# Optimization experiments

Hardware: AMD Instinct MI355X
Metric: run time of the kernel (lower is better)

The kernel has to match this reference:

```python
import jax, jax.numpy as jnp
import numpy as np

B = 2048
BEAMS = 4
DEPTH = 3
HID = 128
NOPS = 4


def _conv(x, w, b):
    y = jax.lax.conv_general_dilated(x, w, (1, 1), 'VALID',
                                     dimension_numbers=('NCHW', 'OIHW', 'NCHW'))
    return y + b[None, :, None, None]


def _bn(x, g, b, eps=1e-5):
    # training-mode BatchNorm2d: batch statistics over (N,H,W)
    mu = x.mean(axis=(0, 2, 3), keepdims=True)
    var = x.var(axis=(0, 2, 3), keepdims=True)
    return (x - mu) * jax.lax.rsqrt(var + eps) * g[None, :, None, None] + b[None, :, None, None]


def _avgpool2(x):
    n, c, h, w = x.shape
    x = x[:, :, :(h // 2) * 2, :(w // 2) * 2]
    return x.reshape(n, c, h // 2, 2, w // 2, 2).mean(axis=(3, 5))


def _backbone(x, cw1, cb1, g1, be1, cw2, cb2, g2, be2, cw3, cb3, g3, be3):
    x = _avgpool2(jax.nn.relu(_bn(_conv(x, cw1, cb1), g1, be1)))  # (N,32,15,15)
    x = _avgpool2(jax.nn.relu(_bn(_conv(x, cw2, cb2), g2, be2)))  # (N,32,6,6)
    x = _avgpool2(jax.nn.relu(_bn(_conv(x, cw3, cb3), g3, be3)))  # (N,32,2,2)
    return x.reshape(x.shape[0], -1)  # (N,128)


def _beam_search(h0, W_hh, b_h, E_op, W_ho, b_ho):
    # tanh-RNN router + top-k beam search over NOPS ops, DEPTH steps.
    # path[t]: (N, BEAMS, NOPS) = one_hot(selected op) * its softmax prob.
    n = h0.shape[0]
    logits0 = h0 @ W_ho + b_ho                       # (N,4)
    logp0 = jax.nn.log_softmax(logits0, axis=-1)
    probs0 = jax.nn.softmax(logits0, axis=-1)
    scores, ops = jax.lax.top_k(logp0, BEAMS)        # (N,beams)
    p = jnp.take_along_axis(probs0, ops, axis=1)
    path = [jax.nn.one_hot(ops, NOPS) * p[..., None]]
    h = jnp.tanh(h0[:, None, :] @ W_hh + E_op[ops] + b_h)  # (N,beams,128)
    for _ in range(DEPTH - 1):
        logits = h @ W_ho + b_ho                     # (N,beams,4)
        logp = jax.nn.log_softmax(logits, axis=-1)
        probs = jax.nn.softmax(logits, axis=-1)
        cand = (scores[:, :, None] + logp).reshape(n, BEAMS * NOPS)
        scores, flat = jax.lax.top_k(cand, BEAMS)
        src = flat // NOPS
        op = flat % NOPS
        probs_src = jnp.take_along_axis(probs, src[:, :, None], axis=1)
        p = jnp.take_along_axis(probs_src, op[:, :, None], axis=2)[..., 0]
        path.append(jax.nn.one_hot(op, NOPS) * p[..., None])
        h_src = jnp.take_along_axis(h, src[:, :, None], axis=1)
        h = jnp.tanh(h_src @ W_hh + E_op[op] + b_h)
    return path


def _dispatch(hid, ops, exp_w, exp_b):
    # per-row argmax-routed expert (3 Linear + Identity), gated by max prob, then ReLU
    idx = jnp.argmax(ops, axis=-1)                   # (M,)
    val = jnp.max(ops, axis=-1)                      # (M,)
    y_lin = jnp.einsum('md,edk->mek', hid, exp_w) + exp_b  # (M,3,128)
    y = jnp.concatenate([y_lin, hid[:, None, :]], axis=1)  # (M,4,128)
    sel = jnp.take_along_axis(y, idx[:, None, None], axis=1)[:, 0]
    return jax.nn.relu(sel * val[:, None])


def _forward(x, cw1, cb1, g1, be1, cw2, cb2, g2, be2, cw3, cb3, g3, be3,
             W_hh, b_h, E_op, W_ho, b_ho, exp_w, exp_b, out_w, out_b):
    h0 = _backbone(x, cw1, cb1, g1, be1, cw2, cb2, g2, be2, cw3, cb3, g3, be3)
    path = _beam_search(h0, W_hh, b_h, E_op, W_ho, b_ho)
    n = h0.shape[0]
    hid = jnp.broadcast_to(h0[:, None, :], (n, BEAMS, HID)).reshape(n * BEAMS, HID)
    for ops in path:
        hid = _dispatch(hid, ops.reshape(n * BEAMS, NOPS), exp_w, exp_b)
    return hid @ out_w + out_b                       # (n*beams, 10)


def setup_inputs():
    key = jax.random.key(0)
    ks = jax.random.split(key, 10)
    s = 0.05
    return {
        'x': jax.random.normal(ks[0], (B, 3, 32, 32), jnp.float32),
        'cw1': jax.random.normal(ks[1], (32, 3, 3, 3), jnp.float32) * s,
        'cb1': jnp.zeros((32,), jnp.float32),
        'g1': jnp.ones((32,), jnp.float32), 'be1': jnp.zeros((32,), jnp.float32),
        'cw2': jax.random.normal(ks[2], (32, 32, 3, 3), jnp.float32) * s,
        'cb2': jnp.zeros((32,), jnp.float32),
        'g2': jnp.ones((32,), jnp.float32), 'be2': jnp.zeros((32,), jnp.float32),
        'cw3': jax.random.normal(ks[3], (32, 32, 3, 3), jnp.float32) * s,
        'cb3': jnp.zeros((32,), jnp.float32),
        'g3': jnp.ones((32,), jnp.float32), 'be3': jnp.zeros((32,), jnp.float32),
        'W_hh': jax.random.normal(ks[4], (HID, HID), jnp.float32) * s,
        'b_h': jnp.zeros((HID,), jnp.float32),
        'E_op': jax.random.normal(ks[5], (NOPS, HID), jnp.float32) * s,
        'W_ho': jax.random.normal(ks[6], (HID, NOPS), jnp.float32) * s,
        'b_ho': jnp.zeros((NOPS,), jnp.float32),
        'exp_w': jax.random.normal(ks[7], (3, HID, HID), jnp.float32) * s,
        'exp_b': jnp.zeros((3, HID), jnp.float32),
        'out_w': jax.random.normal(ks[8], (HID, 10), jnp.float32) * s,
        'out_b': jnp.zeros((10,), jnp.float32),
    }


def reference(x, cw1, cb1, g1, be1, cw2, cb2, g2, be2, cw3, cb3, g3, be3,
              W_hh, b_h, E_op, W_ho, b_ho, exp_w, exp_b, out_w, out_b):
    return _forward(x, cw1, cb1, g1, be1, cw2, cb2, g2, be2, cw3, cb3, g3, be3,
                    W_hh, b_h, E_op, W_ho, b_ho, exp_w, exp_b, out_w, out_b)
```

## Files before the change

### kernel.cpp

```cpp
#include <hip/hip_runtime.h>
#include <cstdint>


static constexpr size_t O_SC    = 0;
static constexpr size_t O_W1T   = 256;
static constexpr size_t O_W2T   = 1152;
static constexpr size_t O_W3T   = 10368;
static constexpr size_t O_SCORES= 19584;
static constexpr size_t O_P0    = 27776;
static constexpr size_t O_P1    = 35968;
static constexpr size_t O_P2    = 44160;
static constexpr size_t O_OP0   = 52352;
static constexpr size_t O_OP1   = 60544;
static constexpr size_t O_OP2   = 68736;
static constexpr size_t O_SRC1  = 76928;
static constexpr size_t O_SRC2  = 85120;
static constexpr size_t O_H0    = 93312;
static constexpr size_t O_H     = 355456;
static constexpr size_t O_H2    = 1404032;
static constexpr size_t O_HIDA  = 2452608;
static constexpr size_t O_HIDB  = 3501184;
static constexpr size_t O_S1P   = 4549760;
static constexpr size_t O_S2C   = 19295360;
static constexpr size_t O_S2P   = 30371968;
static constexpr size_t O_S3C   = 32731264;
static constexpr size_t O_PART  = O_H;
static constexpr size_t O_PART2 = O_H + 131072;

__device__ __forceinline__ int swz8(int Q, int cb) {
    return cb ^ (Q & 7) ^ ((Q >> 3) & 7);
}

__global__ void prep_w(const float* __restrict__ w1, const float* __restrict__ w2,
                       const float* __restrict__ w3, float* __restrict__ w1t,
                       float* __restrict__ w2t, float* __restrict__ w3t) {
    int t = blockIdx.x * 256 + threadIdx.x;
    if (t < 864) {
        int co = t / 27, k = t % 27;
        w1t[k * 32 + co] = w1[t];
    }
    if (t < 9216) {
        int co = t / 288, rest = t % 288;
        int ci = rest / 9, tap = rest % 9;
        int k = tap * 32 + ci;
        w2t[k * 32 + co] = w2[t];
        w3t[k * 32 + co] = w3[t];
    }
}

__global__ __launch_bounds__(256) void reduce_part64(
    const float* __restrict__ part, int nblocks, float* __restrict__ part2) {
    __shared__ float red[256];
    const int b = blockIdx.x, t = threadIdx.x;
    const int c = t & 63, grp = t >> 6;
    float s = 0.f;
    for (int i = b + 64 * grp; i < nblocks; i += 256)
        s += part[(size_t)i * 64 + c];
    red[t] = s;
    __syncthreads();
    if (t < 64)
        part2[(size_t)b * 64 + t] =
            red[t] + red[64 + t] + red[128 + t] + red[192 + t];
}

__global__ __launch_bounds__(256) void finalize_stats(
    const float* __restrict__ part, int nblocks, float invcount,
    const float* __restrict__ g, const float* __restrict__ be,
    float* __restrict__ scsh) {
    __shared__ float red[256];
    const int t = threadIdx.x;
    const int c = t & 63, grp = t >> 6;
    float s = 0.f;
    for (int i = grp; i < nblocks; i += 4) s += part[(size_t)i * 64 + c];
    red[t] = s;
    __syncthreads();
    if (t < 64) red[t] = red[t] + red[64 + t] + red[128 + t] + red[192 + t];
    __syncthreads();
    if (t < 32) {
        float mean = red[t] * invcount;
        float var = red[32 + t] * invcount - mean * mean;
        float sc = g[t] * rsqrtf(var + 1e-5f);
        scsh[t] = sc;
        scsh[32 + t] = be[t] - mean * sc;
    }
}

#define CONV1_STAGE(img4, xin, t)                                              \
    for (int i = (t); i < 1024; i += 256) {                                    \
        int slot = (i & 1) * 16 + ((i & 31) >> 1);                             \
        img4[(i >> 5) * 32 + slot] =                                           \
            make_float4(xin[i], xin[1024 + i], xin[2048 + i], 0.f);            \
    }

__device__ __forceinline__ float f4c(float4 v, int ci) {
    return ci == 0 ? v.x : (ci == 1 ? v.y : v.z);
}

#define CONV1_PQUAD(img4, wb, ph, pw, y)                                       \
    {                                                                          \
        _Pragma("unroll")                                                      \
        for (int tr = 0; tr < 3; ++tr) {                                       \
            const int rb_ = (2 * (ph) + tr) * 32 + (pw);                       \
            float4 a0_[4], a1_[4];                                             \
            a0_[0] = img4[rb_ + 0];  a0_[1] = img4[rb_ + 16];                  \
            a0_[2] = img4[rb_ + 1];  a0_[3] = img4[rb_ + 17];                  \
            a1_[0] = img4[rb_ + 32]; a1_[1] = img4[rb_ + 48];                  \
            a1_[2] = img4[rb_ + 33]; a1_[3] = img4[rb_ + 49];                  \
            _Pragma("unroll")                                                  \
            for (int tc = 0; tc < 3; ++tc) {                                   \
                _Pragma("unroll")                                              \
                for (int ci = 0; ci < 3; ++ci) {                               \
                    const float* w8_ = (wb) + (ci * 9 + tr * 3 + tc) * 32;     \
                    float4 wa_ = *(const float4*)w8_;                          \
                    float4 wq_ = *(const float4*)(w8_ + 4);                    \
                    float wr_[8] = {wa_.x, wa_.y, wa_.z, wa_.w,                \
                                    wq_.x, wq_.y, wq_.z, wq_.w};               \
                    const float s00_ = f4c(a0_[tc], ci);                       \
                    const float s01_ = f4c(a0_[tc + 1], ci);                   \
                    const float s10_ = f4c(a1_[tc], ci);                       \
                    const float s11_ = f4c(a1_[tc + 1], ci);                   \
                    _Pragma("unroll")                                          \
                    for (int cc = 0; cc < 8; ++cc) {                           \
                        y[0][cc] += s00_ * wr_[cc];                            \
                        y[1][cc] += s01_ * wr_[cc];                            \
                        y[2][cc] += s10_ * wr_[cc];                            \
                        y[3][cc] += s11_ * wr_[cc];                            \
                    }                                                          \
                }                                                              \
            }                                                                  \
        }                                                                      \
    }

__global__ __launch_bounds__(256, 4) void conv1_stats_kernel(
    const float* __restrict__ x, const float* __restrict__ w1t,
    float* __restrict__ part) {
    __shared__ float4 img4[1024];
    const int n = blockIdx.x, t = threadIdx.x;
    const float* xin = x + (size_t)n * 3072;
    CONV1_STAGE(img4, xin, t)
    const int wv = t >> 6, lane = t & 63;
    const int c0s = __builtin_amdgcn_readfirstlane(wv * 8);
    const float* __restrict__ wb = w1t + c0s;
    __syncthreads();
    float sm[8] = {}, sq[8] = {};
#pragma unroll 1
    for (int j = 0; j < 4; ++j) {
        const int pp = lane + 64 * j;
        const bool pv = pp < 225;
        const int pc = pv ? pp : 0;
        const int ph = pc / 15, pw = pc % 15;
        float y[4][8] = {};
        CONV1_PQUAD(img4, wb, ph, pw, y)
        if (pv) {
#pragma unroll
            for (int q = 0; q < 4; ++q)
#pragma unroll
                for (int cc = 0; cc < 8; ++cc) {
                    float v = y[q][cc];
                    sm[cc] += v; sq[cc] += v * v;
                }
        }
    }
#pragma unroll
    for (int off = 32; off > 0; off >>= 1)
#pragma unroll
        for (int cc = 0; cc < 8; ++cc) {
            sm[cc] += __shfl_down(sm[cc], off);
            sq[cc] += __shfl_down(sq[cc], off);
        }
    if (lane == 0) {
        float* dst = part + (size_t)n * 64;
#pragma unroll
        for (int cc = 0; cc < 8; ++cc) {
            dst[c0s + cc] = sm[cc];
            dst[32 + c0s + cc] = sq[cc];
        }
    }
}

__global__ __launch_bounds__(256, 4) void conv1_apply_kernel(
    const float* __restrict__ x, const float* __restrict__ w1t,
    const float* __restrict__ scsh, float* __restrict__ s1p) {
    __shared__ float4 img4[1024];
    const int n = blockIdx.x, t = threadIdx.x;
    const float* xin = x + (size_t)n * 3072;
    CONV1_STAGE(img4, xin, t)
    const int wv = t >> 6, lane = t & 63;
    const int c0s = __builtin_amdgcn_readfirstlane(wv * 8);
    const float* __restrict__ wb = w1t + c0s;
    float scv[8], shv[8];
#pragma unroll
    for (int cc = 0; cc < 8; ++cc) {
        scv[cc] = scsh[c0s + cc];
        shv[cc] = scsh[32 + c0s + cc];
    }
    __syncthreads();
#pragma unroll 1
    for (int j = 0; j < 4; ++j) {
        const int pp = lane + 64 * j;
        const bool pv = pp < 225;
        const int pc = pv ? pp : 0;
        const int ph = pc / 15, pw = pc % 15;
        float y[4][8] = {};
        CONV1_PQUAD(img4, wb, ph, pw, y)
        if (pv) {
            float ov[8];
#pragma unroll
            for (int cc = 0; cc < 8; ++cc) {
                float sc = scv[cc], sh = shv[cc];
                float a0 = fmaxf(y[0][cc] * sc + sh, 0.f);
                float a1 = fmaxf(y[1][cc] * sc + sh, 0.f);
                float a2 = fmaxf(y[2][cc] * sc + sh, 0.f);
                float a3 = fmaxf(y[3][cc] * sc + sh, 0.f);
                ov[cc] = 0.25f * (a0 + a1 + a2 + a3);
            }
            float* dst = s1p + ((size_t)n * 225 + pc) * 32 + c0s;
            *(float4*)dst = make_float4(ov[0], ov[1], ov[2], ov[3]);
            *(float4*)(dst + 4) = make_float4(ov[4], ov[5], ov[6], ov[7]);
        }
    }
}

__global__ __launch_bounds__(256, 5) void conv2_kernel(
    const float* __restrict__ s1p, const float* __restrict__ w2t,
    float* __restrict__ s2c, float* __restrict__ part) {
    __shared__ float4 img4[1800];
    const int n = blockIdx.x, t = threadIdx.x;
    const float4* src4 = (const float4*)(s1p + (size_t)n * 7200);
    for (int i = t; i < 1800; i += 256) {
        int p = i >> 3, cb = i & 7;
        img4[(p << 3) + swz8(p, cb)] = src4[i];
    }
    const int wv = t >> 6, lane = t & 63;
    const int c0s = __builtin_amdgcn_readfirstlane(wv * 8);
    const float* __restrict__ wbase = w2t + c0s;
    int pxv[3], in0[3];
    bool val[3];
#pragma unroll
    for (int j = 0; j < 3; ++j) {
        int p = lane + 64 * j;
        val[j] = p < 169;
        int pc = val[j] ? p : 0;
        pxv[j] = pc;
        in0[j] = (pc / 13) * 15 + (pc % 13);
    }
    float y[3][8] = {};
    __syncthreads();
#pragma unroll 1
    for (int tap = 0; tap < 9; ++tap) {
        const int dp = (tap / 3) * 15 + (tap % 3);
        int qb[3], qs[3];
#pragma unroll
        for (int j = 0; j < 3; ++j) {
            int q = in0[j] + dp;
            qb[j] = q << 3;
            qs[j] = (q & 7) ^ ((q >> 3) & 7);
        }
        const float* wk = wbase + tap * 1024;
#pragma unroll
        for (int cb = 0; cb < 8; ++cb) {
            float4 v0 = img4[qb[0] + (cb ^ qs[0])];
            float4 v1 = img4[qb[1] + (cb ^ qs[1])];
            float4 v2 = img4[qb[2] + (cb ^ qs[2])];
#pragma unroll
            for (int u = 0; u < 4; ++u) {
                const float* w8 = wk + (cb * 4 + u) * 32;
                float4 wa = *(const float4*)w8;
                float4 wb = *(const float4*)(w8 + 4);
                float wreg[8] = {wa.x, wa.y, wa.z, wa.w, wb.x, wb.y, wb.z, wb.w};
                float sv[3] = {((const float*)&v0)[u], ((const float*)&v1)[u],
                               ((const float*)&v2)[u]};
#pragma unroll
                for (int j = 0; j < 3; ++j)
#pragma unroll
                    for (int cc = 0; cc < 8; ++cc)
                        y[j][cc] += sv[j] * wreg[cc];
            }
        }
    }
#pragma unroll
    for (int j = 0; j < 3; ++j)
        if (val[j]) {
            float* dst = s2c + ((size_t)n * 169 + pxv[j]) * 32 + c0s;
            *(float4*)dst = make_float4(y[j][0], y[j][1], y[j][2], y[j][3]);
            *(float4*)(dst + 4) = make_float4(y[j][4], y[j][5], y[j][6], y[j][7]);
        }
    float sm[8] = {}, sq[8] = {};
#pragma unroll
    for (int j = 0; j < 3; ++j)
        if (val[j]) {
#pragma unroll
            for (int cc = 0; cc < 8; ++cc) {
                float v = y[j][cc];
                sm[cc] += v; sq[cc] += v * v;
            }
        }
#pragma unroll
    for (int off = 32; off > 0; off >>= 1)
#pragma unroll
        for (int cc = 0; cc < 8; ++cc) {
            sm[cc] += __shfl_down(sm[cc], off);
            sq[cc] += __shfl_down(sq[cc], off);
        }
    if (lane == 0) {
        float* dst = part + (size_t)n * 64;
#pragma unroll
        for (int cc = 0; cc < 8; ++cc) {
            dst[c0s + cc] = sm[cc];
            dst[32 + c0s + cc] = sq[cc];
        }
    }
}

__global__ __launch_bounds__(256) void conv3_kernel(
    const float* __restrict__ s2p, const float* __restrict__ w3t,
    float* __restrict__ s3c, float* __restrict__ part) {
    __shared__ float4 img4[1152];
    const int n0 = blockIdx.x * 4, t = threadIdx.x;
    const float4* src4 = (const float4*)(s2p + (size_t)n0 * 1152);
    for (int i = t; i < 1152; i += 256) {
        int im = i / 288, rem = i - im * 288;
        int p = rem >> 3, cb = rem & 7;
        img4[im * 288 + (p << 3) + swz8(im * 36 + p, cb)] = src4[i];
    }
    const int wv = t >> 6, lane = t & 63;
    const int c0s = __builtin_amdgcn_readfirstlane(wv * 8);
    const float* __restrict__ wbase = w3t + c0s;
    const int im = lane >> 4, p = lane & 15;
    const int in0 = (p >> 2) * 6 + (p & 3);
    float y[8] = {};
    __syncthreads();
#pragma unroll 1
    for (int tap = 0; tap < 9; ++tap) {
        const int q = in0 + (tap / 3) * 6 + (tap % 3);
        const int P = im * 36 + q;
        const int qb = im * 288 + (q << 3);
        const int qs = (P & 7) ^ ((P >> 3) & 7);
        const float* wk = wbase + tap * 1024;
#pragma unroll
        for (int cb = 0; cb < 8; ++cb) {
            float4 v = img4[qb + (cb ^ qs)];
#pragma unroll
            for (int u = 0; u < 4; ++u) {
                const float* w8 = wk + (cb * 4 + u) * 32;
                float4 wa = *(const float4*)w8;
                float4 wb = *(const float4*)(w8 + 4);
                float wreg[8] = {wa.x, wa.y, wa.z, wa.w, wb.x, wb.y, wb.z, wb.w};
                float s = ((const float*)&v)[u];
#pragma unroll
                for (int cc = 0; cc < 8; ++cc) y[cc] += s * wreg[cc];
            }
        }
    }
    float* dst = s3c + ((size_t)(n0 + im) * 16 + p) * 32 + c0s;
    *(float4*)dst = make_float4(y[0], y[1], y[2], y[3]);
    *(float4*)(dst + 4) = make_float4(y[4], y[5], y[6], y[7]);
    float sm[8], sq[8];
#pragma unroll
    for (int cc = 0; cc < 8; ++cc) {
        sm[cc] = y[cc]; sq[cc] = y[cc] * y[cc];
    }
#pragma unroll
    for (int off = 32; off > 0; off >>= 1)
#pragma unroll
        for (int cc = 0; cc < 8; ++cc) {
            sm[cc] += __shfl_down(sm[cc], off);
            sq[cc] += __shfl_down(sq[cc], off);
        }
    if (lane == 0) {
        float* dstp = part + (size_t)blockIdx.x * 64;
#pragma unroll
        for (int cc = 0; cc < 8; ++cc) {
            dstp[c0s + cc] = sm[cc];
            dstp[32 + c0s + cc] = sq[cc];
        }
    }
}

__global__ void bn_pool2(const float* __restrict__ s2c, const float* __restrict__ scsh,
                         float* __restrict__ s2p) {
    __shared__ float bn[64];
    const int t = threadIdx.x;
    if (t < 64) bn[t] = scsh[t];
    __syncthreads();
    for (int idx = blockIdx.x * blockDim.x + t; idx < 2359296;
         idx += gridDim.x * blockDim.x) {
        const int ci = idx & 31, rest = idx >> 5;
        const int pp = rest % 36, n = rest / 36;
        const int ph = pp / 6, pw = pp % 6;
        const float* b = s2c + ((size_t)n * 169 + (2 * ph) * 13 + 2 * pw) * 32 + ci;
        const float s = bn[ci], h = bn[32 + ci];
        float a0 = fmaxf(b[0] * s + h, 0.f);
        float a1 = fmaxf(b[32] * s + h, 0.f);
        float a2 = fmaxf(b[13 * 32] * s + h, 0.f);
        float a3 = fmaxf(b[14 * 32] * s + h, 0.f);
        s2p[idx] = 0.25f * (a0 + a1 + a2 + a3);
    }
}

__global__ void bn_pool3_h0(const float* __restrict__ s3c, const float* __restrict__ scsh,
                            float* __restrict__ h0) {
    __shared__ float bn[64];
    const int t = threadIdx.x;
    if (t < 64) bn[t] = scsh[t];
    __syncthreads();
    const int idx = blockIdx.x * 256 + t;
    if (idx >= 262144) return;
    const int n = idx >> 7, rem = idx & 127;
    const int c = rem >> 2, q = rem & 3, ph = q >> 1, pw = q & 1;
    const float* b = s3c + ((size_t)n * 16 + 2 * ph * 4 + 2 * pw) * 32 + c;
    const float s = bn[c], h = bn[32 + c];
    float a0 = fmaxf(b[0] * s + h, 0.f);
    float a1 = fmaxf(b[32] * s + h, 0.f);
    float a2 = fmaxf(b[128] * s + h, 0.f);
    float a3 = fmaxf(b[160] * s + h, 0.f);
    h0[idx] = 0.25f * (a0 + a1 + a2 + a3);
}

__global__ void beam0_kernel(const float* __restrict__ h0, const float* __restrict__ Who,
                             const float* __restrict__ bho, float* __restrict__ scores,
                             int* __restrict__ op0, float* __restrict__ p0) {
    const int n = blockIdx.x, lane = threadIdx.x;
    const float* hr = h0 + (size_t)n * 128;
    float pt[4] = {};
    for (int i = lane; i < 128; i += 64) {
        float hv = hr[i];
        pt[0] += hv * Who[i * 4 + 0];
        pt[1] += hv * Who[i * 4 + 1];
        pt[2] += hv * Who[i * 4 + 2];
        pt[3] += hv * Who[i * 4 + 3];
    }
#pragma unroll
    for (int off = 32; off > 0; off >>= 1)
#pragma unroll
        for (int o = 0; o < 4; ++o) pt[o] += __shfl_down(pt[o], off);
    if (lane == 0) {
        float lg[4], e[4], probs[4], logp[4];
#pragma unroll
        for (int o = 0; o < 4; ++o) lg[o] = pt[o] + bho[o];
        float m = fmaxf(fmaxf(lg[0], lg[1]), fmaxf(lg[2], lg[3]));
        float sum = 0.f;
#pragma unroll
        for (int o = 0; o < 4; ++o) { e[o] = expf(lg[o] - m); sum += e[o]; }
        float lse = logf(sum);
#pragma unroll
        for (int o = 0; o < 4; ++o) {
            probs[o] = e[o] / sum;
            logp[o] = lg[o] - m - lse;
        }
        bool used[4] = {false, false, false, false};
        for (int slot = 0; slot < 4; ++slot) {
            int best = 0; float bv = -INFINITY;
            for (int o = 0; o < 4; ++o)
                if (!used[o] && logp[o] > bv) { bv = logp[o]; best = o; }
            used[best] = true;
            scores[n * 4 + slot] = bv;
            op0[n * 4 + slot] = best;
            p0[n * 4 + slot] = probs[best];
        }
    }
}

__global__ void beam_level(const float* __restrict__ h, const float* __restrict__ Who,
                           const float* __restrict__ bho, float* __restrict__ scores,
                           int* __restrict__ opL, float* __restrict__ pL,
                           int* __restrict__ srcL) {
    __shared__ float logits[16], cand[16], pr[16];
    const int n = blockIdx.x, l = threadIdx.x;
    const int b = l >> 4, o = (l >> 2) & 3, qt = l & 3;
    const float* hr = h + ((size_t)n * 4 + b) * 128;
    float s = 0.f;
    for (int k = qt * 32; k < qt * 32 + 32; ++k) s += hr[k] * Who[k * 4 + o];
    s += __shfl_xor(s, 1);
    s += __shfl_xor(s, 2);
    if (qt == 0) logits[b * 4 + o] = s + bho[o];
    __syncthreads();
    if (l < 4) {
        float lg[4];
#pragma unroll
        for (int o2 = 0; o2 < 4; ++o2) lg[o2] = logits[l * 4 + o2];
        float m = fmaxf(fmaxf(lg[0], lg[1]), fmaxf(lg[2], lg[3]));
        float e[4], sum = 0.f;
#pragma unroll
        for (int o2 = 0; o2 < 4; ++o2) { e[o2] = expf(lg[o2] - m); sum += e[o2]; }
        float lse = logf(sum);
        float sb = scores[n * 4 + l];
#pragma unroll
        for (int o2 = 0; o2 < 4; ++o2) {
            pr[l * 4 + o2] = e[o2] / sum;
            cand[l * 4 + o2] = sb + (lg[o2] - m - lse);
        }
    }
    __syncthreads();
    if (l == 0) {
        bool used[16];
#pragma unroll
        for (int f = 0; f < 16; ++f) used[f] = false;
        float ns[4], np[4]; int nop[4], nsrc[4];
        for (int slot = 0; slot < 4; ++slot) {
            int best = 0; float bv = -INFINITY;
            for (int f = 0; f < 16; ++f)
                if (!used[f] && cand[f] > bv) { bv = cand[f]; best = f; }
            used[best] = true;
            ns[slot] = bv; nsrc[slot] = best >> 2; nop[slot] = best & 3;
            np[slot] = pr[best];
        }
        for (int slot = 0; slot < 4; ++slot) {
            scores[n * 4 + slot] = ns[slot];
            opL[n * 4 + slot] = nop[slot];
            pL[n * 4 + slot] = np[slot];
            srcL[n * 4 + slot] = nsrc[slot];
        }
    }
}

__global__ __launch_bounds__(256) void h_update(
    const float* __restrict__ in, int mode, const int* __restrict__ srcL,
    const int* __restrict__ opL, const float* __restrict__ Whh,
    const float* __restrict__ Eop, const float* __restrict__ bh,
    float* __restrict__ out) {
    __shared__ float A[256];
    const int r0 = blockIdx.x * 2, t = threadIdx.x;
    const int row = t >> 7, j = t & 127;
    const int r = r0 + row;
    const float* src;
    if (mode == 0) src = in + (size_t)(r >> 2) * 128;
    else           src = in + (size_t)((r & ~3) + srcL[r]) * 128;
    A[t] = src[j];
    __syncthreads();
    float acc = 0.f;
#pragma unroll 8
    for (int k = 0; k < 128; ++k) acc += A[row * 128 + k] * Whh[k * 128 + j];
    out[(size_t)r * 128 + j] = tanhf(acc + Eop[opL[r] * 128 + j] + bh[j]);
}

__global__ __launch_bounds__(256) void dispatch_kernel(
    const float* __restrict__ in, int mode, const int* __restrict__ opL,
    const float* __restrict__ pL, const float* __restrict__ expw,
    const float* __restrict__ expb, float* __restrict__ out) {
    __shared__ float A[256];
    const int r0 = blockIdx.x * 2, t = threadIdx.x;
    const int row = t >> 7, j = t & 127;
    const int r = r0 + row;
    const float* src = (mode == 0) ? in + (size_t)(r >> 2) * 128
                                   : in + (size_t)r * 128;
    A[t] = src[j];
    __syncthreads();
    const int op = opL[r];
    const float p = pL[r];
    float res;
    if (op < 3) {
        const float* Bw = expw + (size_t)op * 16384;
        float acc = 0.f;
#pragma unroll 8
        for (int k = 0; k < 128; ++k) acc += A[row * 128 + k] * Bw[k * 128 + j];
        res = (acc + expb[op * 128 + j]) * p;
    } else {
        res = A[row * 128 + j] * p;
    }
    out[(size_t)r * 128 + j] = fmaxf(res, 0.f);
}

__global__ void final_kernel(const float* __restrict__ hid, const float* __restrict__ ow,
                             const float* __restrict__ ob, float* __restrict__ out) {
    const int idx = blockIdx.x * 256 + threadIdx.x;
    if (idx >= 81920) return;
    const int r = idx / 10, o = idx % 10;
    const float* hr = hid + (size_t)r * 128;
    float acc = ob[o];
#pragma unroll 8
    for (int k = 0; k < 128; ++k) acc += hr[k] * ow[k * 10 + o];
    out[idx] = acc;
}

extern "C" void kernel_launch(void* const* d_in, const int* in_sizes, int n_in,
                              void* d_out, int out_size, void* d_ws, size_t ws_size,
                              hipStream_t stream) {
    const float* x    = (const float*)d_in[0];
    const float* cw1  = (const float*)d_in[1];
    const float* g1   = (const float*)d_in[3];
    const float* be1  = (const float*)d_in[4];
    const float* cw2  = (const float*)d_in[5];
    const float* g2   = (const float*)d_in[7];
    const float* be2  = (const float*)d_in[8];
    const float* cw3  = (const float*)d_in[9];
    const float* g3   = (const float*)d_in[11];
    const float* be3  = (const float*)d_in[12];
    const float* Whh  = (const float*)d_in[13];
    const float* bh   = (const float*)d_in[14];
    const float* Eop  = (const float*)d_in[15];
    const float* Who  = (const float*)d_in[16];
    const float* bho  = (const float*)d_in[17];
    const float* expw = (const float*)d_in[18];
    const float* expb = (const float*)d_in[19];
    const float* outw = (const float*)d_in[20];
    const float* outb = (const float*)d_in[21];
    float* ws  = (float*)d_ws;
    float* out = (float*)d_out;

    prep_w<<<36, 256, 0, stream>>>(cw1, cw2, cw3, ws + O_W1T, ws + O_W2T, ws + O_W3T);

    conv1_stats_kernel<<<2048, 256, 0, stream>>>(x, ws + O_W1T, ws + O_PART);
    reduce_part64<<<64, 256, 0, stream>>>(ws + O_PART, 2048, ws + O_PART2);
    finalize_stats<<<1, 256, 0, stream>>>(ws + O_PART2, 64, 1.f / 1843200.f,
                                          g1, be1, ws + O_SC);
    conv1_apply_kernel<<<2048, 256, 0, stream>>>(x, ws + O_W1T, ws + O_SC, ws + O_S1P);
    conv2_kernel<<<2048, 256, 0, stream>>>(ws + O_S1P, ws + O_W2T, ws + O_S2C,
                                           ws + O_PART);
    reduce_part64<<<64, 256, 0, stream>>>(ws + O_PART, 2048, ws + O_PART2);
    finalize_stats<<<1, 256, 0, stream>>>(ws + O_PART2, 64, 1.f / 346112.f,
                                          g2, be2, ws + O_SC + 64);
    bn_pool2<<<2048, 256, 0, stream>>>(ws + O_S2C, ws + O_SC + 64, ws + O_S2P);
    conv3_kernel<<<512, 256, 0, stream>>>(ws + O_S2P, ws + O_W3T, ws + O_S3C,
                                          ws + O_PART);
    reduce_part64<<<64, 256, 0, stream>>>(ws + O_PART, 512, ws + O_PART2);
    finalize_stats<<<1, 256, 0, stream>>>(ws + O_PART2, 64, 1.f / 32768.f,
                                          g3, be3, ws + O_SC + 128);
    bn_pool3_h0<<<1024, 256, 0, stream>>>(ws + O_S3C, ws + O_SC + 128, ws + O_H0);

    beam0_kernel<<<2048, 64, 0, stream>>>(ws + O_H0, Who, bho, ws + O_SCORES,
                                          (int*)(ws + O_OP0), ws + O_P0);
    h_update<<<4096, 256, 0, stream>>>(ws + O_H0, 0, (int*)(ws + O_SRC2),
                                       (int*)(ws + O_OP0), Whh, Eop, bh, ws + O_H);
    beam_level<<<2048, 64, 0, stream>>>(ws + O_H, Who, bho, ws + O_SCORES,
                                        (int*)(ws + O_OP1), ws + O_P1,
                                        (int*)(ws + O_SRC1));
    h_update<<<4096, 256, 0, stream>>>(ws + O_H, 1, (int*)(ws + O_SRC1),
                                       (int*)(ws + O_OP1), Whh, Eop, bh, ws + O_H2);
    beam_level<<<2048, 64, 0, stream>>>(ws + O_H2, Who, bho, ws + O_SCORES,
                                        (int*)(ws + O_OP2), ws + O_P2,
                                        (int*)(ws + O_SRC2));

    dispatch_kernel<<<4096, 256, 0, stream>>>(ws + O_H0, 0, (int*)(ws + O_OP0),
                                              ws + O_P0, expw, expb, ws + O_HIDA);
    dispatch_kernel<<<4096, 256, 0, stream>>>(ws + O_HIDA, 1, (int*)(ws + O_OP1),
                                              ws + O_P1, expw, expb, ws + O_HIDB);
    dispatch_kernel<<<4096, 256, 0, stream>>>(ws + O_HIDB, 1, (int*)(ws + O_OP2),
                                              ws + O_P2, expw, expb, ws + O_HIDA);
    final_kernel<<<320, 256, 0, stream>>>(ws + O_HIDA, outw, outb, out);
}
```

Baseline: 479.3 us.

## Fuse bn_pool2 into conv3 and merge beam-search levels with RNN and expert steps

Removes the bn_pool2 kernel by having conv3 apply BN2, ReLU and avgpool directly while loading s2c into shared memory. Beam-search top-k is fused into the h_update kernels, with each block recomputing the beam selection for its sample. The last beam level, the third expert dispatch and the final linear layer are merged into one kernel, and conv2's occupancy hint is dropped. This cuts launch count and intermediate global traffic, at the cost of redundant beam computation (each sample is handled by two blocks) and a serial tail on a few threads.

```diff
diff --git a/kernel.cpp b/kernel.cpp
--- a/kernel.cpp
+++ b/kernel.cpp
@@ -9,12 +9,9 @@
 static constexpr size_t O_SCORES= 19584;
 static constexpr size_t O_P0    = 27776;
 static constexpr size_t O_P1    = 35968;
-static constexpr size_t O_P2    = 44160;
+static constexpr size_t O_SC1   = 44160;
 static constexpr size_t O_OP0   = 52352;
 static constexpr size_t O_OP1   = 60544;
-static constexpr size_t O_OP2   = 68736;
-static constexpr size_t O_SRC1  = 76928;
-static constexpr size_t O_SRC2  = 85120;
 static constexpr size_t O_H0    = 93312;
 static constexpr size_t O_H     = 355456;
 static constexpr size_t O_H2    = 1404032;
@@ -22,7 +19,6 @@
 static constexpr size_t O_HIDB  = 3501184;
 static constexpr size_t O_S1P   = 4549760;
 static constexpr size_t O_S2C   = 19295360;
-static constexpr size_t O_S2P   = 30371968;
 static constexpr size_t O_S3C   = 32731264;
 static constexpr size_t O_PART  = O_H;
 static constexpr size_t O_PART2 = O_H + 131072;
@@ -221,7 +217,7 @@
     }
 }
 
-__global__ __launch_bounds__(256, 5) void conv2_kernel(
+__global__ __launch_bounds__(256) void conv2_kernel(
     const float* __restrict__ s1p, const float* __restrict__ w2t,
     float* __restrict__ s2c, float* __restrict__ part) {
     __shared__ float4 img4[1800];
@@ -313,15 +309,36 @@
 }
 
 __global__ __launch_bounds__(256) void conv3_kernel(
-    const float* __restrict__ s2p, const float* __restrict__ w3t,
-    float* __restrict__ s3c, float* __restrict__ part) {
+    const float* __restrict__ s2c, const float* __restrict__ scsh2,
+    const float* __restrict__ w3t, float* __restrict__ s3c,
+    float* __restrict__ part) {
     __shared__ float4 img4[1152];
+    __shared__ float bn2[64];
     const int n0 = blockIdx.x * 4, t = threadIdx.x;
-    const float4* src4 = (const float4*)(s2p + (size_t)n0 * 1152);
+    if (t < 64) bn2[t] = scsh2[t];
+    __syncthreads();
+    const float4* s2c4 = (const float4*)s2c;
     for (int i = t; i < 1152; i += 256) {
         int im = i / 288, rem = i - im * 288;
         int p = rem >> 3, cb = rem & 7;
-        img4[im * 288 + (p << 3) + swz8(im * 36 + p, cb)] = src4[i];
+        int ph = p / 6, pw = p % 6;
+        size_t base = ((size_t)(n0 + im) * 169 + (2 * ph) * 13 + 2 * pw) * 8 + cb;
+        float4 v0 = s2c4[base];
+        float4 v1 = s2c4[base + 8];
+        float4 v2 = s2c4[base + 13 * 8];
+        float4 v3 = s2c4[base + 14 * 8];
+        float4 sc = *(const float4*)&bn2[cb * 4];
+        float4 sh = *(const float4*)&bn2[32 + cb * 4];
+        float4 o;
+        o.x = 0.25f * (fmaxf(v0.x * sc.x + sh.x, 0.f) + fmaxf(v1.x * sc.x + sh.x, 0.f) +
+                       fmaxf(v2.x * sc.x + sh.x, 0.f) + fmaxf(v3.x * sc.x + sh.x, 0.f));
+        o.y = 0.25f * (fmaxf(v0.y * sc.y + sh.y, 0.f) + fmaxf(v1.y * sc.y + sh.y, 0.f) +
+                       fmaxf(v2.y * sc.y + sh.y, 0.f) + fmaxf(v3.y * sc.y + sh.y, 0.f));
+        o.z = 0.25f * (fmaxf(v0.z * sc.z + sh.z, 0.f) + fmaxf(v1.z * sc.z + sh.z, 0.f) +
+                       fmaxf(v2.z * sc.z + sh.z, 0.f) + fmaxf(v3.z * sc.z + sh.z, 0.f));
+        o.w = 0.25f * (fmaxf(v0.w * sc.w + sh.w, 0.f) + fmaxf(v1.w * sc.w + sh.w, 0.f) +
+                       fmaxf(v2.w * sc.w + sh.w, 0.f) + fmaxf(v3.w * sc.w + sh.w, 0.f));
+        img4[im * 288 + (p << 3) + swz8(im * 36 + p, cb)] = o;
     }
     const int wv = t >> 6, lane = t & 63;
     const int c0s = __builtin_amdgcn_readfirstlane(wv * 8);
@@ -374,27 +391,6 @@
             dstp[c0s + cc] = sm[cc];
             dstp[32 + c0s + cc] = sq[cc];
         }
-    }
-}
-
-__global__ void bn_pool2(const float* __restrict__ s2c, const float* __restrict__ scsh,
-                         float* __restrict__ s2p) {
-    __shared__ float bn[64];
-    const int t = threadIdx.x;
-    if (t < 64) bn[t] = scsh[t];
-    __syncthreads();
-    for (int idx = blockIdx.x * blockDim.x + t; idx < 2359296;
-         idx += gridDim.x * blockDim.x) {
-        const int ci = idx & 31, rest = idx >> 5;
-        const int pp = rest % 36, n = rest / 36;
-        const int ph = pp / 6, pw = pp % 6;
-        const float* b = s2c + ((size_t)n * 169 + (2 * ph) * 13 + 2 * pw) * 32 + ci;
-        const float s = bn[ci], h = bn[32 + ci];
-        float a0 = fmaxf(b[0] * s + h, 0.f);
-        float a1 = fmaxf(b[32] * s + h, 0.f);
-        float a2 = fmaxf(b[13 * 32] * s + h, 0.f);
-        float a3 = fmaxf(b[14 * 32] * s + h, 0.f);
-        s2p[idx] = 0.25f * (a0 + a1 + a2 + a3);
     }
 }
 
@@ -417,121 +413,132 @@
     h0[idx] = 0.25f * (a0 + a1 + a2 + a3);
 }
 
-__global__ void beam0_kernel(const float* __restrict__ h0, const float* __restrict__ Who,
-                             const float* __restrict__ bho, float* __restrict__ scores,
-                             int* __restrict__ op0, float* __restrict__ p0) {
-    const int n = blockIdx.x, lane = threadIdx.x;
-    const float* hr = h0 + (size_t)n * 128;
-    float pt[4] = {};
-    for (int i = lane; i < 128; i += 64) {
-        float hv = hr[i];
-        pt[0] += hv * Who[i * 4 + 0];
-        pt[1] += hv * Who[i * 4 + 1];
-        pt[2] += hv * Who[i * 4 + 2];
-        pt[3] += hv * Who[i * 4 + 3];
-    }
-#pragma unroll
-    for (int off = 32; off > 0; off >>= 1)
-#pragma unroll
-        for (int o = 0; o < 4; ++o) pt[o] += __shfl_down(pt[o], off);
-    if (lane == 0) {
-        float lg[4], e[4], probs[4], logp[4];
-#pragma unroll
-        for (int o = 0; o < 4; ++o) lg[o] = pt[o] + bho[o];
-        float m = fmaxf(fmaxf(lg[0], lg[1]), fmaxf(lg[2], lg[3]));
-        float sum = 0.f;
-#pragma unroll
-        for (int o = 0; o < 4; ++o) { e[o] = expf(lg[o] - m); sum += e[o]; }
-        float lse = logf(sum);
-#pragma unroll
-        for (int o = 0; o < 4; ++o) {
-            probs[o] = e[o] / sum;
-            logp[o] = lg[o] - m - lse;
-        }
-        bool used[4] = {false, false, false, false};
-        for (int slot = 0; slot < 4; ++slot) {
-            int best = 0; float bv = -INFINITY;
-            for (int o = 0; o < 4; ++o)
-                if (!used[o] && logp[o] > bv) { bv = logp[o]; best = o; }
-            used[best] = true;
-            scores[n * 4 + slot] = bv;
-            op0[n * 4 + slot] = best;
-            p0[n * 4 + slot] = probs[best];
-        }
-    }
-}
-
-__global__ void beam_level(const float* __restrict__ h, const float* __restrict__ Who,
-                           const float* __restrict__ bho, float* __restrict__ scores,
-                           int* __restrict__ opL, float* __restrict__ pL,
-                           int* __restrict__ srcL) {
+__global__ __launch_bounds__(256) void beam0_h_fused(
+    const float* __restrict__ h0, const float* __restrict__ Who,
+    const float* __restrict__ bho, const float* __restrict__ Whh,
+    const float* __restrict__ Eop, const float* __restrict__ bhv,
+    float* __restrict__ scores0, int* __restrict__ op0, float* __restrict__ p0,
+    float* __restrict__ hout) {
+    __shared__ float A[256];
+    __shared__ int s_op[4];
+    const int blk = blockIdx.x, t = threadIdx.x;
+    const int n = blk >> 1;
+    if (t < 64) {
+        const float* hr = h0 + (size_t)n * 128;
+        float pt[4] = {};
+        for (int i = t; i < 128; i += 64) {
+            float hv = hr[i];
+            pt[0] += hv * Who[i * 4 + 0];
+            pt[1] += hv * Who[i * 4 + 1];
+            pt[2] += hv * Who[i * 4 + 2];
+            pt[3] += hv * Who[i * 4 + 3];
+        }
+#pragma unroll
+        for (int off = 32; off > 0; off >>= 1)
+#pragma unroll
+            for (int o = 0; o < 4; ++o) pt[o] += __shfl_down(pt[o], off);
+        if (t == 0) {
+            float lg[4], e[4], probs[4], logp[4];
+#pragma unroll
+            for (int o = 0; o < 4; ++o) lg[o] = pt[o] + bho[o];
+            float m = fmaxf(fmaxf(lg[0], lg[1]), fmaxf(lg[2], lg[3]));
+            float sum = 0.f;
+#pragma unroll
+            for (int o = 0; o < 4; ++o) { e[o] = expf(lg[o] - m); sum += e[o]; }
+            float lse = logf(sum);
+#pragma unroll
+            for (int o = 0; o < 4; ++o) {
+                probs[o] = e[o] / sum;
+                logp[o] = lg[o] - m - lse;
+            }
+            bool used[4] = {false, false, false, false};
+            for (int slot = 0; slot < 4; ++slot) {
+                int best = 0; float bv = -INFINITY;
+                for (int o = 0; o < 4; ++o)
+                    if (!used[o] && logp[o] > bv) { bv = logp[o]; best = o; }
+                used[best] = true;
+                scores0[n * 4 + slot] = bv;
+                op0[n * 4 + slot] = best;
+                p0[n * 4 + slot] = probs[best];
+                s_op[slot] = best;
+            }
+        }
+    }
+    __syncthreads();
+    const int row = t >> 7, j = t & 127;
+    const int r = blk * 2 + row;
+    A[t] = h0[(size_t)n * 128 + j];
+    __syncthreads();
+    float acc = 0.f;
+#pragma unroll 8
+    for (int k = 0; k < 128; ++k) acc += A[row * 128 + k] * Whh[k * 128 + j];
+    const int op = s_op[r & 3];
+    hout[(size_t)r * 128 + j] = tanhf(acc + Eop[op * 128 + j] + bhv[j]);
+}
+
+__global__ __launch_bounds__(256) void lvl_h_fused(
+    const float* __restrict__ h, const float* __restrict__ Who,
+    const float* __restrict__ bho, const float* __restrict__ scores_in,
+    const float* __restrict__ Whh, const float* __restrict__ Eop,
+    const float* __restrict__ bhv, float* __restrict__ scores_out,
+    int* __restrict__ opL, float* __restrict__ pL, float* __restrict__ hout) {
     __shared__ float logits[16], cand[16], pr[16];
-    const int n = blockIdx.x, l = threadIdx.x;
-    const int b = l >> 4, o = (l >> 2) & 3, qt = l & 3;
-    const float* hr = h + ((size_t)n * 4 + b) * 128;
-    float s = 0.f;
-    for (int k = qt * 32; k < qt * 32 + 32; ++k) s += hr[k] * Who[k * 4 + o];
-    s += __shfl_xor(s, 1);
-    s += __shfl_xor(s, 2);
-    if (qt == 0) logits[b * 4 + o] = s + bho[o];
-    __syncthreads();
-    if (l < 4) {
+    __shared__ int s_op[4], s_src[4];
+    __shared__ float A[256];
+    const int blk = blockIdx.x, t = threadIdx.x;
+    const int n = blk >> 1;
+    if (t < 64) {
+        const int b = t >> 4, o = (t >> 2) & 3, qt = t & 3;
+        const float* hr = h + ((size_t)n * 4 + b) * 128;
+        float s = 0.f;
+        for (int k = qt * 32; k < qt * 32 + 32; ++k) s += hr[k] * Who[k * 4 + o];
+        s += __shfl_xor(s, 1);
+        s += __shfl_xor(s, 2);
+        if (qt == 0) logits[b * 4 + o] = s + bho[o];
+    }
+    __syncthreads();
+    if (t < 4) {
         float lg[4];
 #pragma unroll
-        for (int o2 = 0; o2 < 4; ++o2) lg[o2] = logits[l * 4 + o2];
+        for (int o2 = 0; o2 < 4; ++o2) lg[o2] = logits[t * 4 + o2];
         float m = fmaxf(fmaxf(lg[0], lg[1]), fmaxf(lg[2], lg[3]));
         float e[4], sum = 0.f;
 #pragma unroll
         for (int o2 = 0; o2 < 4; ++o2) { e[o2] = expf(lg[o2] - m); sum += e[o2]; }
         float lse = logf(sum);
-        float sb = scores[n * 4 + l];
+        float sb = scores_in[n * 4 + t];
 #pragma unroll
         for (int o2 = 0; o2 < 4; ++o2) {
-            pr[l * 4 + o2] = e[o2] / sum;
-            cand[l * 4 + o2] = sb + (lg[o2] - m - lse);
-        }
-    }
-    __syncthreads();
-    if (l == 0) {
+            pr[t * 4 + o2] = e[o2] / sum;
+            cand[t * 4 + o2] = sb + (lg[o2] - m - lse);
+        }
+    }
+    __syncthreads();
+    if (t == 0) {
         bool used[16];
 #pragma unroll
         for (int f = 0; f < 16; ++f) used[f] = false;
-        float ns[4], np[4]; int nop[4], nsrc[4];
         for (int slot = 0; slot < 4; ++slot) {
             int best = 0; float bv = -INFINITY;
             for (int f = 0; f < 16; ++f)
                 if (!used[f] && cand[f] > bv) { bv = cand[f]; best = f; }
             used[best] = true;
-            ns[slot] = bv; nsrc[slot] = best >> 2; nop[slot] = best & 3;
-            np[slot] = pr[best];
-        }
-        for (int slot = 0; slot < 4; ++slot) {
-            scores[n * 4 + slot] = ns[slot];
-            opL[n * 4 + slot] = nop[slot];
-            pL[n * 4 + slot] = np[slot];
-            srcL[n * 4 + slot] = nsrc[slot];
-        }
-    }
-}
-
-__global__ __launch_bounds__(256) void h_update(
-    const float* __restrict__ in, int mode, const int* __restrict__ srcL,
-    const int* __restrict__ opL, const float* __restrict__ Whh,
-    const float* __restrict__ Eop, const float* __restrict__ bh,
-    float* __restrict__ out) {
-    __shared__ float A[256];
-    const int r0 = blockIdx.x * 2, t = threadIdx.x;
+            scores_out[n * 4 + slot] = bv;
+            opL[n * 4 + slot] = best & 3;
+            pL[n * 4 + slot] = pr[best];
+            s_op[slot] = best & 3;
+            s_src[slot] = best >> 2;
+        }
+    }
+    __syncthreads();
     const int row = t >> 7, j = t & 127;
-    const int r = r0 + row;
-    const float* src;
-    if (mode == 0) src = in + (size_t)(r >> 2) * 128;
-    else           src = in + (size_t)((r & ~3) + srcL[r]) * 128;
-    A[t] = src[j];
+    const int r = blk * 2 + row;
+    A[t] = h[((size_t)(r & ~3) + s_src[r & 3]) * 128 + j];
     __syncthreads();
     float acc = 0.f;
 #pragma unroll 8
     for (int k = 0; k < 128; ++k) acc += A[row * 128 + k] * Whh[k * 128 + j];
-    out[(size_t)r * 128 + j] = tanhf(acc + Eop[opL[r] * 128 + j] + bh[j]);
+    hout[(size_t)r * 128 + j] = tanhf(acc + Eop[s_op[r & 3] * 128 + j] + bhv[j]);
 }
 
 __global__ __launch_bounds__(256) void dispatch_kernel(
@@ -561,16 +568,85 @@
     out[(size_t)r * 128 + j] = fmaxf(res, 0.f);
 }
 
-__global__ void final_kernel(const float* __restrict__ hid, const float* __restrict__ ow,
-                             const float* __restrict__ ob, float* __restrict__ out) {
-    const int idx = blockIdx.x * 256 + threadIdx.x;
-    if (idx >= 81920) return;
-    const int r = idx / 10, o = idx % 10;
-    const float* hr = hid + (size_t)r * 128;
-    float acc = ob[o];
+__global__ __launch_bounds__(256) void lvl2_d3_final_fused(
+    const float* __restrict__ h2, const float* __restrict__ Who,
+    const float* __restrict__ bho, const float* __restrict__ scores_in,
+    const float* __restrict__ hidin, const float* __restrict__ expw,
+    const float* __restrict__ expb, const float* __restrict__ ow,
+    const float* __restrict__ ob, float* __restrict__ outp) {
+    __shared__ float logits[16], cand[16], pr[16];
+    __shared__ int s_op[4];
+    __shared__ float s_p[4];
+    __shared__ float A[256], B[256];
+    const int blk = blockIdx.x, t = threadIdx.x;
+    const int n = blk >> 1;
+    if (t < 64) {
+        const int b = t >> 4, o = (t >> 2) & 3, qt = t & 3;
+        const float* hr = h2 + ((size_t)n * 4 + b) * 128;
+        float s = 0.f;
+        for (int k = qt * 32; k < qt * 32 + 32; ++k) s += hr[k] * Who[k * 4 + o];
+        s += __shfl_xor(s, 1);
+        s += __shfl_xor(s, 2);
+        if (qt == 0) logits[b * 4 + o] = s + bho[o];
+    }
+    __syncthreads();
+    if (t < 4) {
+        float lg[4];
+#pragma unroll
+        for (int o2 = 0; o2 < 4; ++o2) lg[o2] = logits[t * 4 + o2];
+        float m = fmaxf(fmaxf(lg[0], lg[1]), fmaxf(lg[2], lg[3]));
+        float e[4], sum = 0.f;
+#pragma unroll
+        for (int o2 = 0; o2 < 4; ++o2) { e[o2] = expf(lg[o2] - m); sum += e[o2]; }
+        float lse = logf(sum);
+        float sb = scores_in[n * 4 + t];
+#pragma unroll
+        for (int o2 = 0; o2 < 4; ++o2) {
+            pr[t * 4 + o2] = e[o2] / sum;
+            cand[t * 4 + o2] = sb + (lg[o2] - m - lse);
+        }
+    }
+    __syncthreads();
+    if (t == 0) {
+        bool used[16];
+#pragma unroll
+        for (int f = 0; f < 16; ++f) used[f] = false;
+        for (int slot = 0; slot < 4; ++slot) {
+            int best = 0; float bv = -INFINITY;
+            for (int f = 0; f < 16; ++f)
+                if (!used[f] && cand[f] > bv) { bv = cand[f]; best = f; }
+            used[best] = true;
+            s_op[slot] = best & 3;
+            s_p[slot] = pr[best];
+        }
+    }
+    __syncthreads();
+    const int row = t >> 7, j = t & 127;
+    const int r = blk * 2 + row;
+    A[t] = hidin[(size_t)r * 128 + j];
+    __syncthreads();
+    const int op = s_op[r & 3];
+    const float p = s_p[r & 3];
+    float res;
+    if (op < 3) {
+        const float* Bw = expw + (size_t)op * 16384;
+        float acc = 0.f;
 #pragma unroll 8
-    for (int k = 0; k < 128; ++k) acc += hr[k] * ow[k * 10 + o];
-    out[idx] = acc;
+        for (int k = 0; k < 128; ++k) acc += A[row * 128 + k] * Bw[k * 128 + j];
+        res = (acc + expb[op * 128 + j]) * p;
+    } else {
+        res = A[row * 128 + j] * p;
+    }
+    B[t] = fmaxf(res, 0.f);
+    __syncthreads();
+    if (t < 20) {
+        const int row2 = t / 10, o = t % 10;
+        const int rr = blk * 2 + row2;
+        float acc = ob[o];
+#pragma unroll 8
+        for (int k = 0; k < 128; ++k) acc += B[row2 * 128 + k] * ow[k * 10 + o];
+        outp[rr * 10 + o] = acc;
+    }
 }
 
 extern "C" void kernel_launch(void* const* d_in, const int* in_sizes, int n_in,
@@ -610,32 +686,24 @@
     reduce_part64<<<64, 256, 0, stream>>>(ws + O_PART, 2048, ws + O_PART2);
     finalize_stats<<<1, 256, 0, stream>>>(ws + O_PART2, 64, 1.f / 346112.f,
                                           g2, be2, ws + O_SC + 64);
-    bn_pool2<<<2048, 256, 0, stream>>>(ws + O_S2C, ws + O_SC + 64, ws + O_S2P);
-    conv3_kernel<<<512, 256, 0, stream>>>(ws + O_S2P, ws + O_W3T, ws + O_S3C,
-                                          ws + O_PART);
+    conv3_kernel<<<512, 256, 0, stream>>>(ws + O_S2C, ws + O_SC + 64, ws + O_W3T,
+                                          ws + O_S3C, ws + O_PART);
     reduce_part64<<<64, 256, 0, stream>>>(ws + O_PART, 512, ws + O_PART2);
     finalize_stats<<<1, 256, 0, stream>>>(ws + O_PART2, 64, 1.f / 32768.f,
                                           g3, be3, ws + O_SC + 128);
     bn_pool3_h0<<<1024, 256, 0, stream>>>(ws + O_S3C, ws + O_SC + 128, ws + O_H0);
 
-    beam0_kernel<<<2048, 64, 0, stream>>>(ws + O_H0, Who, bho, ws + O_SCORES,
-                                          (int*)(ws + O_OP0), ws + O_P0);
-    h_update<<<4096, 256, 0, stream>>>(ws + O_H0, 0, (int*)(ws + O_SRC2),
-                                       (int*)(ws + O_OP0), Whh, Eop, bh, ws + O_H);
-    beam_level<<<2048, 64, 0, stream>>>(ws + O_H, Who, bho, ws + O_SCORES,
-                                        (int*)(ws + O_OP1), ws + O_P1,
-                                        (int*)(ws + O_SRC1));
-    h_update<<<4096, 256, 0, stream>>>(ws + O_H, 1, (int*)(ws + O_SRC1),
-                                       (int*)(ws + O_OP1), Whh, Eop, bh, ws + O_H2);
-    beam_level<<<2048, 64, 0, stream>>>(ws + O_H2, Who, bho, ws + O_SCORES,
-                                        (int*)(ws + O_OP2), ws + O_P2,
-                                        (int*)(ws + O_SRC2));
-
+    beam0_h_fused<<<4096, 256, 0, stream>>>(ws + O_H0, Who, bho, Whh, Eop, bh,
+                                            ws + O_SCORES, (int*)(ws + O_OP0),
+                                            ws + O_P0, ws + O_H);
     dispatch_kernel<<<4096, 256, 0, stream>>>(ws + O_H0, 0, (int*)(ws + O_OP0),
                                               ws + O_P0, expw, expb, ws + O_HIDA);
+    lvl_h_fused<<<4096, 256, 0, stream>>>(ws + O_H, Who, bho, ws + O_SCORES,
+                                          Whh, Eop, bh, ws + O_SC1,
+                                          (int*)(ws + O_OP1), ws + O_P1, ws + O_H2);
     dispatch_kernel<<<4096, 256, 0, stream>>>(ws + O_HIDA, 1, (int*)(ws + O_OP1),
                                               ws + O_P1, expw, expb, ws + O_HIDB);
-    dispatch_kernel<<<4096, 256, 0, stream>>>(ws + O_HIDB, 1, (int*)(ws + O_OP2),
-                                              ws + O_P2, expw, expb, ws + O_HIDA);
-    final_kernel<<<320, 256, 0, stream>>>(ws + O_HIDA, outw, outb, out);
-}
+    lvl2_d3_final_fused<<<4096, 256, 0, stream>>>(ws + O_H2, Who, bho, ws + O_SC1,
+                                                  ws + O_HIDB, expw, expb,
+                                                  outw, outb, out);
+}
```

New measurement: 496.4 us, median of 3. 3.6% more time.
